# Kernel optimization log

Measured on AMD Instinct MI355X. Metric: run time of the kernel, lower is better.

Reference implementation:

```python
import jax, jax.numpy as jnp
import numpy as np

K_PRESERVE = 256
NUM_NEW = 1
UNITS = 768
HEAD_DIM = 64
N_HEADS = UNITS // HEAD_DIM
HID = 768


def setup_inputs() -> dict:
    key = jax.random.key(0)
    ks = jax.random.split(key, 12)
    B, H, L, D = 32, 12, 512, HID
    s = 0.02
    return {
        "hidden_states": jax.random.normal(ks[0], (B, L, D), jnp.float32),
        "attention_mask": jnp.zeros((B, 1, 1, L), jnp.float32),
        "self_attention_scores": jax.random.normal(ks[1], (B, H, L, L), jnp.float32),
        "Wq": jax.random.normal(ks[2], (D, UNITS), jnp.float32) * s,
        "bq": jnp.zeros((UNITS,), jnp.float32),
        "Wk": jax.random.normal(ks[3], (D, UNITS), jnp.float32) * s,
        "bk": jnp.zeros((UNITS,), jnp.float32),
        "Wv": jax.random.normal(ks[4], (D, UNITS), jnp.float32) * s,
        "bv": jnp.zeros((UNITS,), jnp.float32),
        "Wo": jax.random.normal(ks[5], (UNITS, D), jnp.float32) * s,
        "bo": jnp.zeros((D,), jnp.float32),
    }


def _forward(hidden_states, attention_mask, self_attention_scores,
             Wq, bq, Wk, bk, Wv, bv, Wo, bo):
    B, L, D = hidden_states.shape
    # K after reserving the new token slot
    K = max(min(K_PRESERVE, L) - NUM_NEW, 1)

    am = attention_mask.reshape(B, L)                      # additive mask as [B,L]
    amf = (am > -10.0).astype(jnp.float32)
    elem = amf[:, :, None] * amf[:, None, :]               # [B,L,L]
    scores = self_attention_scores * elem[:, None, :, :]   # [B,H,L,L]

    imp = scores.mean(axis=1).mean(axis=1)                 # [B,L]
    imp = imp.at[:, 0].set(jnp.inf)                        # always keep CLS
    _, idx = jax.lax.top_k(imp, K)                         # [B,K]
    idx = jnp.sort(idx, axis=-1)                           # boolean-mask gather keeps order

    preserved = jnp.take_along_axis(hidden_states, idx[:, :, None], axis=1)  # [B,K,D]
    preserved_mask = jnp.take_along_axis(am, idx, axis=1).reshape(B, 1, 1, K)

    # sentence vector = softmax(mask) @ hidden
    att = jax.nn.softmax(am, axis=-1)                      # [B,L]
    sentences = jnp.einsum('bl,bld->bd', att, hidden_states)[:, None, :]  # [B,1,D]
    key_pad = am < -10.0                                    # [B,L] True = masked

    # small cross-attention producing one new token
    q = (sentences @ Wq + bq).reshape(B, 1, N_HEADS, HEAD_DIM)
    k = (hidden_states @ Wk + bk).reshape(B, L, N_HEADS, HEAD_DIM)
    v = (hidden_states @ Wv + bv).reshape(B, L, N_HEADS, HEAD_DIM)
    logits = jnp.einsum('bqhd,blhd->bhql', q, k) / np.sqrt(HEAD_DIM).astype(np.float32)
    logits = jnp.where(key_pad[:, None, None, :], -jnp.inf, logits)
    w = jax.nn.softmax(logits, axis=-1)                    # [B,H,1,L]
    ctx = jnp.einsum('bhql,blhd->bqhd', w, v).reshape(B, 1, UNITS)
    new_token = ctx @ Wo + bo                              # [B,1,D]

    final_token = jnp.concatenate([preserved, new_token], axis=1)         # [B,K+1,D]
    new_mask = jnp.zeros((B, 1, 1, 1), jnp.float32)
    final_mask = jnp.concatenate([preserved_mask, new_mask], axis=-1)     # [B,1,1,K+1]
    tome_size = jnp.ones((B, K + 1, 1), jnp.float32)
    return final_token, final_mask, tome_size


def reference(hidden_states, attention_mask, self_attention_scores,
              Wq, bq, Wk, bk, Wv, bv, Wo, bo):
    return _forward(hidden_states, attention_mask, self_attention_scores,
                    Wq, bq, Wk, bk, Wv, bv, Wo, bo)
```

## Files before the change

### kernel.cpp

```cpp
#include <hip/hip_runtime.h>
#include <cstdint>
#include <cstddef>

#define B 32
#define H 12
#define L 512
#define D 768
#define KSEL 255

#define OFF_IMP   0
#define MEMSET_BYTES 65536
#define OFF_ATT   65536
#define OFF_SENT  131072
#define OFF_Q     229376
#define OFF_CB    327680
#define OFF_A     329216
#define OFF_LG    1508864
#define OFF_SEL   2295296
#define OFF_Y     2327936
#define OFF_CTX   3507584

__device__ __forceinline__ void imp_slice(const float* __restrict__ sas,
                                          const float* __restrict__ am,
                                          float* __restrict__ imp,
                                          int vb, int t, float4* red) {
  const int b = vb / 48, r = vb % 48, h = r >> 2, ch = r & 3;
  const int g = t >> 7, c = t & 127;
  const int row0 = ch * 128 + g * 32;
  const float* base = sas + (((size_t)(b * H + h)) * L + row0) * L;
  const float* amb = am + b * L + row0;
  float a0 = 0, a1 = 0, a2 = 0, a3 = 0;
#pragma unroll 8
  for (int l = 0; l < 32; ++l) {
    const float m = (amb[l] > -10.0f) ? 1.0f : 0.0f;
    const float4 v = reinterpret_cast<const float4*>(base + (size_t)l * L)[c];
    a0 += m * v.x;
    a1 += m * v.y;
    a2 += m * v.z;
    a3 += m * v.w;
  }
  red[g * 128 + c] = make_float4(a0, a1, a2, a3);
  __syncthreads();
  if (g == 0) {
    const float4 r0 = red[c], r1 = red[128 + c], r2 = red[256 + c], r3 = red[384 + c];
    float* ip = imp + b * L + c * 4;
    atomicAdd(ip + 0, r0.x + r1.x + r2.x + r3.x);
    atomicAdd(ip + 1, r0.y + r1.y + r2.y + r3.y);
    atomicAdd(ip + 2, r0.z + r1.z + r2.z + r3.z);
    atomicAdd(ip + 3, r0.w + r1.w + r2.w + r3.w);
  }
}

__global__ __launch_bounds__(512) void k_f1(const float* __restrict__ sas,
                                            const float* __restrict__ am,
                                            float* __restrict__ imp,
                                            float* __restrict__ att,
                                            float* __restrict__ sent) {
  __shared__ float4 red[512];
  __shared__ float r1[8], r2[8];
  const int bid = blockIdx.x, t = threadIdx.x;
  imp_slice(sas, am, imp, bid, t, red);
  if (bid < B) {
    const int b = bid, l = t;
    sent[b * D + l] = 0.0f;
    if (l < D - 512) sent[b * D + 512 + l] = 0.0f;
    const float aml = am[b * L + l];
    float m = aml;
#pragma unroll
    for (int o = 32; o; o >>= 1) m = fmaxf(m, __shfl_down(m, o));
    if ((l & 63) == 0) r1[l >> 6] = m;
    __syncthreads();
    if (l == 0) {
      float mm = r1[0];
      for (int i = 1; i < 8; ++i) mm = fmaxf(mm, r1[i]);
      r1[0] = mm;
    }
    __syncthreads();
    const float M = r1[0];
    const float e = expf(aml - M);
    float s = e;
#pragma unroll
    for (int o = 32; o; o >>= 1) s += __shfl_down(s, o);
    if ((l & 63) == 0) r2[l >> 6] = s;
    __syncthreads();
    if (l == 0) {
      float ss = 0.f;
      for (int i = 0; i < 8; ++i) ss += r2[i];
      r2[0] = ss;
    }
    __syncthreads();
    att[b * L + l] = e / r2[0];
  }
}

__global__ __launch_bounds__(512) void k_f2(const float* __restrict__ sas,
                                            const float* __restrict__ am,
                                            const float* __restrict__ hs,
                                            const float* __restrict__ att,
                                            float* __restrict__ imp,
                                            float* __restrict__ sent) {
  __shared__ float4 red[512];
  __shared__ float a[64];
  __shared__ float4 red2[8][192];
  const int bid = blockIdx.x, t = threadIdx.x;
  imp_slice(sas, am, imp, 512 + bid, t, red);
  if (bid < 256) {
    const int b = bid >> 3, c = bid & 7;
    const int w = t >> 6, lane = t & 63;
    if (t < 64) a[t] = att[b * L + c * 64 + t];
    __syncthreads();
    const float* h0 = hs + ((size_t)b * L + c * 64) * D;
    float4 s0 = {0, 0, 0, 0}, s1 = {0, 0, 0, 0}, s2 = {0, 0, 0, 0};
    for (int l = w; l < 64; l += 8) {
      const float al = a[l];
      const float4* row = reinterpret_cast<const float4*>(h0 + (size_t)l * D);
      const float4 v0 = row[lane], v1 = row[lane + 64], v2 = row[lane + 128];
      s0.x += al * v0.x; s0.y += al * v0.y; s0.z += al * v0.z; s0.w += al * v0.w;
      s1.x += al * v1.x; s1.y += al * v1.y; s1.z += al * v1.z; s1.w += al * v1.w;
      s2.x += al * v2.x; s2.y += al * v2.y; s2.z += al * v2.z; s2.w += al * v2.w;
    }
    red2[w][lane] = s0;
    red2[w][lane + 64] = s1;
    red2[w][lane + 128] = s2;
    __syncthreads();
    if (t < 192) {
      float4 s = {0, 0, 0, 0};
#pragma unroll
      for (int ww = 0; ww < 8; ++ww) {
        const float4 u = red2[ww][t];
        s.x += u.x; s.y += u.y; s.z += u.z; s.w += u.w;
      }
      float* sp = sent + b * D + t * 4;
      atomicAdd(sp + 0, s.x);
      atomicAdd(sp + 1, s.y);
      atomicAdd(sp + 2, s.z);
      atomicAdd(sp + 3, s.w);
    }
  }
}

__global__ __launch_bounds__(512) void k_f3(const float* __restrict__ sas,
                                            const float* __restrict__ am,
                                            const float* __restrict__ sent,
                                            const float* __restrict__ Wq,
                                            const float* __restrict__ bq,
                                            const float* __restrict__ bk,
                                            float* __restrict__ imp,
                                            float* __restrict__ qg,
                                            float* __restrict__ cbg,
                                            float* __restrict__ y) {
  __shared__ float4 red[512];
  const int bid = blockIdx.x, t = threadIdx.x;
  imp_slice(sas, am, imp, 1024 + bid, t, red);
  if (bid < 48) {
    const int h = bid >> 2;
    const int b = (bid & 3) * 8 + (t >> 6);
    const int ul = t & 63;
    const int u = h * 64 + ul;
    const float* sb = sent + b * D;
    float a0 = 0.f, a1 = 0.f, a2 = 0.f, a3 = 0.f;
#pragma unroll 4
    for (int d = 0; d < D; d += 4) {
      a0 += sb[d + 0] * Wq[(size_t)(d + 0) * D + u];
      a1 += sb[d + 1] * Wq[(size_t)(d + 1) * D + u];
      a2 += sb[d + 2] * Wq[(size_t)(d + 2) * D + u];
      a3 += sb[d + 3] * Wq[(size_t)(d + 3) * D + u];
    }
    const float acc = bq[u] + ((a0 + a1) + (a2 + a3));
    qg[b * D + u] = acc;
    float v = bk[u] * acc;
#pragma unroll
    for (int o = 32; o; o >>= 1) v += __shfl_down(v, o);
    if (ul == 0) cbg[b * H + h] = v;
  } else if (bid < 80) {
    const int b = bid - 48;
    for (int i = t; i < H * D; i += 512) y[(size_t)b * H * D + i] = 0.0f;
  }
}

__global__ __launch_bounds__(512) void k_f4(const float* __restrict__ am,
                                            const float* __restrict__ imp,
                                            const float* __restrict__ qg,
                                            const float* __restrict__ Wk,
                                            int* __restrict__ sel,
                                            float* __restrict__ out_mask,
                                            float* __restrict__ out_tome,
                                            float* __restrict__ Ag) {
  const int bid = blockIdx.x, t = threadIdx.x;
  __shared__ float v[512];
  __shared__ int sc[512];
  __shared__ float tile[64][65];
  if (bid < B) {
    const int b = bid, l = t;
    const float aml = am[b * L + l];
    float val;
    if (l == 0)
      val = INFINITY;
    else
      val = (aml > -10.0f) ? imp[b * L + l] : 0.0f;
    v[l] = val;
    __syncthreads();
    int r = 0;
    for (int tt = 0; tt < 512; ++tt) {
      const float vt = v[tt];
      r += (vt > val) || (vt == val && tt < l);
    }
    const int f = (r < KSEL) ? 1 : 0;
    sc[l] = f;
    __syncthreads();
    for (int off = 1; off < 512; off <<= 1) {
      const int add = (l >= off) ? sc[l - off] : 0;
      __syncthreads();
      sc[l] += add;
      __syncthreads();
    }
    if (f) {
      const int pos = sc[l] - 1;
      sel[b * KSEL + pos] = l;
      out_mask[b * 256 + pos] = aml;
    }
    if (l == 0) out_mask[b * 256 + 255] = 0.0f;
    if (l < 256) out_tome[b * 256 + l] = 1.0f;
  } else {
    const int vb = bid - B;
    const int h = vb / 12, dc = vb % 12;
    for (int i = t; i < 4096; i += 512) {
      const int rr = i >> 6, cc = i & 63;
      tile[rr][cc] = Wk[(size_t)(dc * 64 + rr) * D + h * 64 + cc];
    }
    __syncthreads();
    const int dl = t & 63, bl = t >> 6;
    const int d = dc * 64 + dl;
#pragma unroll
    for (int pass = 0; pass < 4; ++pass) {
      const int b = pass * 8 + bl;
      const float* qh = qg + b * D + h * 64;
      float acc = 0.f;
#pragma unroll
      for (int c = 0; c < 64; ++c) acc += tile[dl][c] * qh[c];
      Ag[((size_t)b * H + h) * D + d] = acc;
    }
  }
}

__global__ __launch_bounds__(256) void k_f5(const float* __restrict__ hs,
                                            const float* __restrict__ Ag,
                                            const float* __restrict__ cbg,
                                            const int* __restrict__ sel,
                                            float* __restrict__ lg,
                                            float* __restrict__ out_tok) {
  const int bid = blockIdx.x, t = threadIdx.x;
  __shared__ float A[H * D];
  if (bid < 512) {
    const int b = bid >> 4, ch = bid & 15;
    for (int i = t; i < H * D; i += 256) A[i] = Ag[(size_t)b * H * D + i];
    __syncthreads();
    const int wave = t >> 6, lane = t & 63;
    const float* h0 = hs + (size_t)b * L * D;
    for (int li = 0; li < 8; ++li) {
      const int l = ch * 32 + li * 4 + wave;
      const float* xr = h0 + (size_t)l * D;
      float xv[12];
#pragma unroll
      for (int k = 0; k < 12; ++k) xv[k] = xr[lane + 64 * k];
#pragma unroll
      for (int h = 0; h < H; ++h) {
        float a = 0.f;
#pragma unroll
        for (int k = 0; k < 12; ++k) a += xv[k] * A[h * D + lane + 64 * k];
#pragma unroll
        for (int o = 32; o; o >>= 1) a += __shfl_down(a, o);
        if (lane == 0) lg[((size_t)b * H + h) * L + l] = (a + cbg[b * H + h]) * 0.125f;
      }
    }
  } else {
    const int vb = bid - 512;
    const int row = vb * 4 + (t >> 6);
    const int lane = t & 63;
    const int b = row / KSEL, p = row % KSEL;
    const int j = sel[row];
    const float4* src = reinterpret_cast<const float4*>(hs + ((size_t)b * L + j) * D);
    float4* dst = reinterpret_cast<float4*>(out_tok + ((size_t)b * 256 + p) * D);
#pragma unroll
    for (int i = 0; i < 3; ++i) dst[lane + 64 * i] = src[lane + 64 * i];
  }
}

__global__ __launch_bounds__(768) void k_ysoft(const float* __restrict__ hs,
                                               const float* __restrict__ lg,
                                               const float* __restrict__ am,
                                               float* __restrict__ y) {
  const int b = blockIdx.x, c = blockIdx.y, t = threadIdx.x;
  __shared__ float wl[H * L];
  __shared__ float Ms[H], Is[H];
  __shared__ float wn[H * 64];
  for (int i = t; i < H * L; i += 768) {
    const int l = i & (L - 1);
    const float aml = am[b * L + l];
    wl[i] = (aml < -10.0f) ? -INFINITY : lg[(size_t)b * H * L + i];
  }
  __syncthreads();
  {
    const int h = t >> 6, lane = t & 63;
    float m = -INFINITY;
#pragma unroll
    for (int k = 0; k < 8; ++k) m = fmaxf(m, wl[h * L + lane + 64 * k]);
#pragma unroll
    for (int o = 32; o; o >>= 1) m = fmaxf(m, __shfl_xor(m, o));
    float s = 0.f;
#pragma unroll
    for (int k = 0; k < 8; ++k) s += expf(wl[h * L + lane + 64 * k] - m);
#pragma unroll
    for (int o = 32; o; o >>= 1) s += __shfl_xor(s, o);
    if (lane == 0) { Ms[h] = m; Is[h] = 1.0f / s; }
  }
  __syncthreads();
  {
    const int h = t >> 6, l = t & 63;
    wn[t] = expf(wl[h * L + c * 64 + l] - Ms[h]) * Is[h];
  }
  __syncthreads();
  const float* h0 = hs + ((size_t)b * L + c * 64) * D;
  float acc[12];
#pragma unroll
  for (int h = 0; h < 12; ++h) acc[h] = 0.f;
  for (int l = 0; l < 64; ++l) {
    const float x = h0[(size_t)l * D + t];
#pragma unroll
    for (int h = 0; h < 12; ++h) acc[h] += wn[h * 64 + l] * x;
  }
#pragma unroll
  for (int h = 0; h < 12; ++h) atomicAdd(&y[((size_t)b * H + h) * D + t], acc[h]);
}

__global__ __launch_bounds__(512) void k_ctx(const float* __restrict__ y,
                                             const float* __restrict__ Wv,
                                             const float* __restrict__ bv,
                                             float* __restrict__ ctx) {
  const int h = blockIdx.x;
  const int b = blockIdx.y * 8 + (threadIdx.x >> 6);
  const int c = threadIdx.x & 63;
  const float* yb = y + ((size_t)b * H + h) * D;
  float a0 = 0.f, a1 = 0.f, a2 = 0.f, a3 = 0.f;
#pragma unroll 4
  for (int d = 0; d < D; d += 4) {
    a0 += yb[d + 0] * Wv[(size_t)(d + 0) * D + h * 64 + c];
    a1 += yb[d + 1] * Wv[(size_t)(d + 1) * D + h * 64 + c];
    a2 += yb[d + 2] * Wv[(size_t)(d + 2) * D + h * 64 + c];
    a3 += yb[d + 3] * Wv[(size_t)(d + 3) * D + h * 64 + c];
  }
  ctx[b * D + h * 64 + c] = bv[h * 64 + c] + ((a0 + a1) + (a2 + a3));
}

__global__ __launch_bounds__(512) void k_out(const float* __restrict__ ctx,
                                             const float* __restrict__ Wo,
                                             const float* __restrict__ bo,
                                             float* __restrict__ out_tok) {
  const int dc = blockIdx.x;
  const int b = blockIdx.y * 8 + (threadIdx.x >> 6);
  const int dl = threadIdx.x & 63;
  const int dd = dc * 64 + dl;
  const float* cb = ctx + b * D;
  float a0 = 0.f, a1 = 0.f, a2 = 0.f, a3 = 0.f;
#pragma unroll 4
  for (int u = 0; u < D; u += 4) {
    a0 += cb[u + 0] * Wo[(size_t)(u + 0) * D + dd];
    a1 += cb[u + 1] * Wo[(size_t)(u + 1) * D + dd];
    a2 += cb[u + 2] * Wo[(size_t)(u + 2) * D + dd];
    a3 += cb[u + 3] * Wo[(size_t)(u + 3) * D + dd];
  }
  out_tok[((size_t)b * 256 + 255) * D + dd] = bo[dd] + ((a0 + a1) + (a2 + a3));
}

extern "C" void kernel_launch(void* const* d_in, const int* in_sizes, int n_in,
                              void* d_out, int out_size, void* d_ws, size_t ws_size,
                              hipStream_t stream) {
  const float* hs = (const float*)d_in[0];
  const float* am = (const float*)d_in[1];
  const float* sas = (const float*)d_in[2];
  const float* Wq = (const float*)d_in[3];
  const float* bq = (const float*)d_in[4];
  const float* Wk = (const float*)d_in[5];
  const float* bk = (const float*)d_in[6];
  const float* Wv = (const float*)d_in[7];
  const float* bv = (const float*)d_in[8];
  const float* Wo = (const float*)d_in[9];
  const float* bo = (const float*)d_in[10];

  float* out_tok = (float*)d_out;
  float* out_mask = out_tok + (size_t)B * 256 * D;
  float* out_tome = out_mask + (size_t)B * 256;

  char* ws = (char*)d_ws;
  float* imp = (float*)(ws + OFF_IMP);
  float* att = (float*)(ws + OFF_ATT);
  float* sent = (float*)(ws + OFF_SENT);
  float* qg = (float*)(ws + OFF_Q);
  float* cbg = (float*)(ws + OFF_CB);
  float* Ag = (float*)(ws + OFF_A);
  float* lg = (float*)(ws + OFF_LG);
  int* sel = (int*)(ws + OFF_SEL);
  float* yg = (float*)(ws + OFF_Y);
  float* ctx = (float*)(ws + OFF_CTX);

  hipMemsetAsync(d_ws, 0, MEMSET_BYTES, stream);

  k_f1<<<512, 512, 0, stream>>>(sas, am, imp, att, sent);
  k_f2<<<512, 512, 0, stream>>>(sas, am, hs, att, imp, sent);
  k_f3<<<512, 512, 0, stream>>>(sas, am, sent, Wq, bq, bk, imp, qg, cbg, yg);
  k_f4<<<176, 512, 0, stream>>>(am, imp, qg, Wk, sel, out_mask, out_tome, Ag);
  k_f5<<<2552, 256, 0, stream>>>(hs, Ag, cbg, sel, lg, out_tok);
  k_ysoft<<<dim3(B, 8), 768, 0, stream>>>(hs, lg, am, yg);
  k_ctx<<<dim3(12, 4), 512, 0, stream>>>(yg, Wv, bv, ctx);
  k_out<<<dim3(12, 4), 512, 0, stream>>>(ctx, Wo, bo, out_tok);
}
```

Measured before the change: 751.3 us.

## Merge all stages into one cooperative persistent kernel with grid syncs

Replaces the memset and eight separate kernel launches with a single cooperative kernel of 256 blocks of 768 threads that uses grid-wide syncs between phases. The importance reduction over the score tensor is re-tiled per (batch, head) and interleaved with the sentence-vector and Q/A projections. The ctx and output projections are fused per batch through shared memory. This removes launch gaps and inter-kernel bubbles, but restricts parallelism to 256 resident blocks and adds grid-sync overhead, which may underuse bandwidth on the large score read.

```diff
diff --git a/kernel.cpp b/kernel.cpp
--- a/kernel.cpp
+++ b/kernel.cpp
@@ -1,37 +1,47 @@
 #include <hip/hip_runtime.h>
+#include <hip/hip_cooperative_groups.h>
 #include <cstdint>
 #include <cstddef>
+
+namespace cg = cooperative_groups;
 
 #define B 32
 #define H 12
 #define L 512
 #define D 768
 #define KSEL 255
+#define GN 256
+#define NT 768
 
 #define OFF_IMP   0
-#define MEMSET_BYTES 65536
-#define OFF_ATT   65536
-#define OFF_SENT  131072
-#define OFF_Q     229376
-#define OFF_CB    327680
-#define OFF_A     329216
-#define OFF_LG    1508864
-#define OFF_SEL   2295296
-#define OFF_Y     2327936
-#define OFF_CTX   3507584
-
-__device__ __forceinline__ void imp_slice(const float* __restrict__ sas,
-                                          const float* __restrict__ am,
-                                          float* __restrict__ imp,
-                                          int vb, int t, float4* red) {
-  const int b = vb / 48, r = vb % 48, h = r >> 2, ch = r & 3;
+#define OFF_SENT  65536
+#define OFF_Y     163840
+#define ZERO_F4   83968
+#define OFF_CB    1343488
+#define OFF_A     1345024
+#define OFF_LG    2524672
+#define OFF_SEL   3311104
+
+union ShMem {
+  struct { float4 red[768]; } imp;
+  struct { float4 red2[12][192]; float r1[8]; float r2[8]; float a[64]; } sent;
+  struct { float qpart[12][64]; float q_s[64]; } qa;
+  struct { float v[512]; int sc[512]; } prep;
+  struct { float wl[H * L]; float Ms[H]; float Is[H]; float wn[NT]; } ys;
+  struct { float c[D]; } ctxout;
+};
+
+__device__ __forceinline__ void imp_vb(const float* __restrict__ sas,
+                                       const float* __restrict__ am,
+                                       float* __restrict__ imp,
+                                       int vb, int t, float4* red) {
+  const int b = vb / H, h = vb % H;
   const int g = t >> 7, c = t & 127;
-  const int row0 = ch * 128 + g * 32;
-  const float* base = sas + (((size_t)(b * H + h)) * L + row0) * L;
-  const float* amb = am + b * L + row0;
-  float a0 = 0, a1 = 0, a2 = 0, a3 = 0;
-#pragma unroll 8
-  for (int l = 0; l < 32; ++l) {
+  const float* base = sas + ((size_t)(b * H + h)) * L * L;
+  const float* amb = am + b * L;
+  float a0 = 0.f, a1 = 0.f, a2 = 0.f, a3 = 0.f;
+#pragma unroll 4
+  for (int l = g; l < L; l += 6) {
     const float m = (amb[l] > -10.0f) ? 1.0f : 0.0f;
     const float4 v = reinterpret_cast<const float4*>(base + (size_t)l * L)[c];
     a0 += m * v.x;
@@ -39,337 +49,300 @@
     a2 += m * v.z;
     a3 += m * v.w;
   }
-  red[g * 128 + c] = make_float4(a0, a1, a2, a3);
+  red[t] = make_float4(a0, a1, a2, a3);
   __syncthreads();
   if (g == 0) {
-    const float4 r0 = red[c], r1 = red[128 + c], r2 = red[256 + c], r3 = red[384 + c];
+    float4 s = red[c];
+#pragma unroll
+    for (int gg = 1; gg < 6; ++gg) {
+      const float4 u = red[gg * 128 + c];
+      s.x += u.x; s.y += u.y; s.z += u.z; s.w += u.w;
+    }
     float* ip = imp + b * L + c * 4;
-    atomicAdd(ip + 0, r0.x + r1.x + r2.x + r3.x);
-    atomicAdd(ip + 1, r0.y + r1.y + r2.y + r3.y);
-    atomicAdd(ip + 2, r0.z + r1.z + r2.z + r3.z);
-    atomicAdd(ip + 3, r0.w + r1.w + r2.w + r3.w);
-  }
-}
-
-__global__ __launch_bounds__(512) void k_f1(const float* __restrict__ sas,
-                                            const float* __restrict__ am,
-                                            float* __restrict__ imp,
-                                            float* __restrict__ att,
-                                            float* __restrict__ sent) {
-  __shared__ float4 red[512];
-  __shared__ float r1[8], r2[8];
+    atomicAdd(ip + 0, s.x);
+    atomicAdd(ip + 1, s.y);
+    atomicAdd(ip + 2, s.z);
+    atomicAdd(ip + 3, s.w);
+  }
+  __syncthreads();
+}
+
+__device__ __forceinline__ void sent_unit(const float* __restrict__ am,
+                                          const float* __restrict__ hs,
+                                          float* __restrict__ sent,
+                                          int u, int t, ShMem& sh) {
+  const int b = u >> 3, c = u & 7;
+  const int w = t >> 6, lane = t & 63;
+  const float aml = (t < L) ? am[b * L + t] : -INFINITY;
+  float m = aml;
+#pragma unroll
+  for (int o = 32; o; o >>= 1) m = fmaxf(m, __shfl_down(m, o));
+  if (t < L && lane == 0) sh.sent.r1[w] = m;
+  __syncthreads();
+  if (t == 0) {
+    float mm = sh.sent.r1[0];
+    for (int i = 1; i < 8; ++i) mm = fmaxf(mm, sh.sent.r1[i]);
+    sh.sent.r1[0] = mm;
+  }
+  __syncthreads();
+  const float M = sh.sent.r1[0];
+  const float e = (t < L) ? expf(aml - M) : 0.f;
+  float s = e;
+#pragma unroll
+  for (int o = 32; o; o >>= 1) s += __shfl_down(s, o);
+  if (t < L && lane == 0) sh.sent.r2[w] = s;
+  __syncthreads();
+  if (t == 0) {
+    float ss = 0.f;
+    for (int i = 0; i < 8; ++i) ss += sh.sent.r2[i];
+    sh.sent.r2[0] = ss;
+  }
+  __syncthreads();
+  const float S = sh.sent.r2[0];
+  if (t >= c * 64 && t < c * 64 + 64) sh.sent.a[t - c * 64] = e / S;
+  __syncthreads();
+  const float* h0 = hs + ((size_t)b * L + c * 64) * D;
+  float4 s0 = {0, 0, 0, 0}, s1 = {0, 0, 0, 0}, s2 = {0, 0, 0, 0};
+  for (int l = w; l < 64; l += 12) {
+    const float al = sh.sent.a[l];
+    const float4* row = reinterpret_cast<const float4*>(h0 + (size_t)l * D);
+    const float4 v0 = row[lane], v1 = row[lane + 64], v2 = row[lane + 128];
+    s0.x += al * v0.x; s0.y += al * v0.y; s0.z += al * v0.z; s0.w += al * v0.w;
+    s1.x += al * v1.x; s1.y += al * v1.y; s1.z += al * v1.z; s1.w += al * v1.w;
+    s2.x += al * v2.x; s2.y += al * v2.y; s2.z += al * v2.z; s2.w += al * v2.w;
+  }
+  sh.sent.red2[w][lane] = s0;
+  sh.sent.red2[w][lane + 64] = s1;
+  sh.sent.red2[w][lane + 128] = s2;
+  __syncthreads();
+  if (t < 192) {
+    float4 acc = {0, 0, 0, 0};
+#pragma unroll
+    for (int ww = 0; ww < 12; ++ww) {
+      const float4 uu = sh.sent.red2[ww][t];
+      acc.x += uu.x; acc.y += uu.y; acc.z += uu.z; acc.w += uu.w;
+    }
+    float* sp = sent + b * D + t * 4;
+    atomicAdd(sp + 0, acc.x);
+    atomicAdd(sp + 1, acc.y);
+    atomicAdd(sp + 2, acc.z);
+    atomicAdd(sp + 3, acc.w);
+  }
+  __syncthreads();
+}
+
+__device__ __forceinline__ void qa_unit(const float* __restrict__ sent,
+                                        const float* __restrict__ Wq,
+                                        const float* __restrict__ bq,
+                                        const float* __restrict__ bk,
+                                        const float* __restrict__ Wk,
+                                        float* __restrict__ cbg,
+                                        float* __restrict__ Ag,
+                                        int u, int t, ShMem& sh) {
+  const int b = u / H, h = u % H;
+  const int w = t >> 6, lane = t & 63;
+  const float* sb = sent + b * D;
+  const float* wq = Wq + (size_t)(w * 64) * D + h * 64 + lane;
+  float acc = 0.f;
+#pragma unroll 8
+  for (int dd = 0; dd < 64; ++dd) acc += sb[w * 64 + dd] * wq[(size_t)dd * D];
+  sh.qa.qpart[w][lane] = acc;
+  __syncthreads();
+  if (t < 64) {
+    float q = bq[h * 64 + t];
+#pragma unroll
+    for (int ww = 0; ww < 12; ++ww) q += sh.qa.qpart[ww][t];
+    sh.qa.q_s[t] = q;
+  }
+  __syncthreads();
+  if (t < 64) {
+    float v = bk[h * 64 + t] * sh.qa.q_s[t];
+#pragma unroll
+    for (int o = 32; o; o >>= 1) v += __shfl_down(v, o);
+    if (t == 0) cbg[b * H + h] = v;
+  }
+  const float4* wkrow = reinterpret_cast<const float4*>(Wk + (size_t)t * D + h * 64);
+  float a0 = 0.f, a1 = 0.f, a2 = 0.f, a3 = 0.f;
+#pragma unroll
+  for (int cc = 0; cc < 16; ++cc) {
+    const float4 wv = wkrow[cc];
+    a0 += wv.x * sh.qa.q_s[cc * 4 + 0];
+    a1 += wv.y * sh.qa.q_s[cc * 4 + 1];
+    a2 += wv.z * sh.qa.q_s[cc * 4 + 2];
+    a3 += wv.w * sh.qa.q_s[cc * 4 + 3];
+  }
+  Ag[((size_t)b * H + h) * D + t] = (a0 + a1) + (a2 + a3);
+  __syncthreads();
+}
+
+__global__ __launch_bounds__(NT, 3) void k_mega(
+    const float* __restrict__ hs, const float* __restrict__ am,
+    const float* __restrict__ sas,
+    const float* __restrict__ Wq, const float* __restrict__ bq,
+    const float* __restrict__ Wk, const float* __restrict__ bk,
+    const float* __restrict__ Wv, const float* __restrict__ bv,
+    const float* __restrict__ Wo, const float* __restrict__ bo,
+    float* __restrict__ imp, float* __restrict__ sent, float* __restrict__ y,
+    float* __restrict__ cbg, float* __restrict__ Ag, float* __restrict__ lg,
+    int* __restrict__ sel, float* __restrict__ out_tok,
+    float* __restrict__ out_mask, float* __restrict__ out_tome) {
+  cg::grid_group grid = cg::this_grid();
+  __shared__ ShMem sh;
   const int bid = blockIdx.x, t = threadIdx.x;
-  imp_slice(sas, am, imp, bid, t, red);
+
+  {
+    const int gtid = bid * NT + t;
+    float4* zz = reinterpret_cast<float4*>(imp);
+    if (gtid < ZERO_F4) zz[gtid] = make_float4(0.f, 0.f, 0.f, 0.f);
+    if (gtid < B * 256) out_tome[gtid] = 1.0f;
+    if (gtid < B) out_mask[gtid * 256 + 255] = 0.0f;
+  }
+  grid.sync();
+
+  if (bid < 192) {
+    imp_vb(sas, am, imp, bid, t, sh.imp.red);
+  } else {
+    for (int k = 0; k < 4; ++k) sent_unit(am, hs, sent, (bid - 192) + 64 * k, t, sh);
+  }
+  grid.sync();
+
+  if (bid >= 64) {
+    imp_vb(sas, am, imp, 192 + (bid - 64), t, sh.imp.red);
+  } else {
+    for (int k = 0; k < 6; ++k) qa_unit(sent, Wq, bq, bk, Wk, cbg, Ag, bid + 64 * k, t, sh);
+  }
+  grid.sync();
+
   if (bid < B) {
-    const int b = bid, l = t;
-    sent[b * D + l] = 0.0f;
-    if (l < D - 512) sent[b * D + 512 + l] = 0.0f;
-    const float aml = am[b * L + l];
-    float m = aml;
-#pragma unroll
-    for (int o = 32; o; o >>= 1) m = fmaxf(m, __shfl_down(m, o));
-    if ((l & 63) == 0) r1[l >> 6] = m;
-    __syncthreads();
-    if (l == 0) {
-      float mm = r1[0];
-      for (int i = 1; i < 8; ++i) mm = fmaxf(mm, r1[i]);
-      r1[0] = mm;
-    }
-    __syncthreads();
-    const float M = r1[0];
-    const float e = expf(aml - M);
-    float s = e;
-#pragma unroll
-    for (int o = 32; o; o >>= 1) s += __shfl_down(s, o);
-    if ((l & 63) == 0) r2[l >> 6] = s;
-    __syncthreads();
-    if (l == 0) {
-      float ss = 0.f;
-      for (int i = 0; i < 8; ++i) ss += r2[i];
-      r2[0] = ss;
-    }
-    __syncthreads();
-    att[b * L + l] = e / r2[0];
-  }
-}
-
-__global__ __launch_bounds__(512) void k_f2(const float* __restrict__ sas,
-                                            const float* __restrict__ am,
-                                            const float* __restrict__ hs,
-                                            const float* __restrict__ att,
-                                            float* __restrict__ imp,
-                                            float* __restrict__ sent) {
-  __shared__ float4 red[512];
-  __shared__ float a[64];
-  __shared__ float4 red2[8][192];
-  const int bid = blockIdx.x, t = threadIdx.x;
-  imp_slice(sas, am, imp, 512 + bid, t, red);
-  if (bid < 256) {
+    const int b = bid;
+    float aml = 0.f, val = 0.f;
+    if (t < L) {
+      aml = am[b * L + t];
+      val = (t == 0) ? INFINITY : ((aml > -10.0f) ? imp[b * L + t] : 0.0f);
+      sh.prep.v[t] = val;
+    }
+    __syncthreads();
+    int r = 0;
+    if (t < L) {
+      for (int tt = 0; tt < L; ++tt) {
+        const float vt = sh.prep.v[tt];
+        r += (vt > val) || (vt == val && tt < t);
+      }
+      sh.prep.sc[t] = (r < KSEL) ? 1 : 0;
+    }
+    const int f = (t < L) && (r < KSEL);
+    __syncthreads();
+    for (int off = 1; off < L; off <<= 1) {
+      int add = 0;
+      if (t < L && t >= off) add = sh.prep.sc[t - off];
+      __syncthreads();
+      if (t < L) sh.prep.sc[t] += add;
+      __syncthreads();
+    }
+    if (f) {
+      const int pos = sh.prep.sc[t] - 1;
+      sel[b * KSEL + pos] = t;
+      out_mask[b * 256 + pos] = aml;
+    }
+  } else {
+    const int h = t >> 6, lane = t & 63;
+    for (int u = bid - 32; u < B * 16; u += 224) {
+      const int b = u >> 4, ch = u & 15;
+      const float cbh = cbg[b * H + h];
+      float Areg[12];
+#pragma unroll
+      for (int k = 0; k < 12; ++k) Areg[k] = Ag[((size_t)b * H + h) * D + lane + 64 * k];
+      const float* h0 = hs + (size_t)b * L * D;
+      for (int li = 0; li < 32; ++li) {
+        const int l = ch * 32 + li;
+        const float* xr = h0 + (size_t)l * D;
+        float a = 0.f;
+#pragma unroll
+        for (int k = 0; k < 12; ++k) a += xr[lane + 64 * k] * Areg[k];
+#pragma unroll
+        for (int o = 32; o; o >>= 1) a += __shfl_down(a, o);
+        if (lane == 0) lg[((size_t)b * H + h) * L + l] = (a + cbh) * 0.125f;
+      }
+    }
+  }
+  grid.sync();
+
+  {
     const int b = bid >> 3, c = bid & 7;
+    for (int i = t; i < H * L; i += NT) {
+      const int l = i & (L - 1);
+      const float aml = am[b * L + l];
+      sh.ys.wl[i] = (aml < -10.0f) ? -INFINITY : lg[(size_t)b * H * L + i];
+    }
+    __syncthreads();
+    {
+      const int h = t >> 6, lane = t & 63;
+      float m = -INFINITY;
+#pragma unroll
+      for (int k = 0; k < 8; ++k) m = fmaxf(m, sh.ys.wl[h * L + lane + 64 * k]);
+#pragma unroll
+      for (int o = 32; o; o >>= 1) m = fmaxf(m, __shfl_xor(m, o));
+      float s = 0.f;
+#pragma unroll
+      for (int k = 0; k < 8; ++k) s += expf(sh.ys.wl[h * L + lane + 64 * k] - m);
+#pragma unroll
+      for (int o = 32; o; o >>= 1) s += __shfl_xor(s, o);
+      if (lane == 0) { sh.ys.Ms[h] = m; sh.ys.Is[h] = 1.0f / s; }
+    }
+    __syncthreads();
+    {
+      const int h = t >> 6, l = t & 63;
+      sh.ys.wn[t] = expf(sh.ys.wl[h * L + c * 64 + l] - sh.ys.Ms[h]) * sh.ys.Is[h];
+    }
+    __syncthreads();
+    const float* h0 = hs + ((size_t)b * L + c * 64) * D;
+    float acc[12];
+#pragma unroll
+    for (int h = 0; h < 12; ++h) acc[h] = 0.f;
+    for (int l = 0; l < 64; ++l) {
+      const float x = h0[(size_t)l * D + t];
+#pragma unroll
+      for (int h = 0; h < 12; ++h) acc[h] += sh.ys.wn[h * 64 + l] * x;
+    }
+#pragma unroll
+    for (int h = 0; h < 12; ++h) atomicAdd(&y[((size_t)b * H + h) * D + t], acc[h]);
+  }
+  {
     const int w = t >> 6, lane = t & 63;
-    if (t < 64) a[t] = att[b * L + c * 64 + t];
-    __syncthreads();
-    const float* h0 = hs + ((size_t)b * L + c * 64) * D;
-    float4 s0 = {0, 0, 0, 0}, s1 = {0, 0, 0, 0}, s2 = {0, 0, 0, 0};
-    for (int l = w; l < 64; l += 8) {
-      const float al = a[l];
-      const float4* row = reinterpret_cast<const float4*>(h0 + (size_t)l * D);
-      const float4 v0 = row[lane], v1 = row[lane + 64], v2 = row[lane + 128];
-      s0.x += al * v0.x; s0.y += al * v0.y; s0.z += al * v0.z; s0.w += al * v0.w;
-      s1.x += al * v1.x; s1.y += al * v1.y; s1.z += al * v1.z; s1.w += al * v1.w;
-      s2.x += al * v2.x; s2.y += al * v2.y; s2.z += al * v2.z; s2.w += al * v2.w;
-    }
-    red2[w][lane] = s0;
-    red2[w][lane + 64] = s1;
-    red2[w][lane + 128] = s2;
-    __syncthreads();
-    if (t < 192) {
-      float4 s = {0, 0, 0, 0};
-#pragma unroll
-      for (int ww = 0; ww < 8; ++ww) {
-        const float4 u = red2[ww][t];
-        s.x += u.x; s.y += u.y; s.z += u.z; s.w += u.w;
-      }
-      float* sp = sent + b * D + t * 4;
-      atomicAdd(sp + 0, s.x);
-      atomicAdd(sp + 1, s.y);
-      atomicAdd(sp + 2, s.z);
-      atomicAdd(sp + 3, s.w);
-    }
-  }
-}
-
-__global__ __launch_bounds__(512) void k_f3(const float* __restrict__ sas,
-                                            const float* __restrict__ am,
-                                            const float* __restrict__ sent,
-                                            const float* __restrict__ Wq,
-                                            const float* __restrict__ bq,
-                                            const float* __restrict__ bk,
-                                            float* __restrict__ imp,
-                                            float* __restrict__ qg,
-                                            float* __restrict__ cbg,
-                                            float* __restrict__ y) {
-  __shared__ float4 red[512];
-  const int bid = blockIdx.x, t = threadIdx.x;
-  imp_slice(sas, am, imp, 1024 + bid, t, red);
-  if (bid < 48) {
-    const int h = bid >> 2;
-    const int b = (bid & 3) * 8 + (t >> 6);
-    const int ul = t & 63;
-    const int u = h * 64 + ul;
-    const float* sb = sent + b * D;
+    for (int rr = bid * 12 + w; rr < B * KSEL; rr += GN * 12) {
+      const int b2 = rr / KSEL, p = rr % KSEL;
+      const int j = sel[rr];
+      const float4* src = reinterpret_cast<const float4*>(hs + ((size_t)b2 * L + j) * D);
+      float4* dst = reinterpret_cast<float4*>(out_tok + ((size_t)b2 * 256 + p) * D);
+#pragma unroll
+      for (int i = 0; i < 3; ++i) dst[lane + 64 * i] = src[lane + 64 * i];
+    }
+  }
+  grid.sync();
+
+  if (bid < B) {
+    const int b = bid;
+    const float* yh = y + ((size_t)b * H + (t >> 6)) * D;
     float a0 = 0.f, a1 = 0.f, a2 = 0.f, a3 = 0.f;
 #pragma unroll 4
     for (int d = 0; d < D; d += 4) {
-      a0 += sb[d + 0] * Wq[(size_t)(d + 0) * D + u];
-      a1 += sb[d + 1] * Wq[(size_t)(d + 1) * D + u];
-      a2 += sb[d + 2] * Wq[(size_t)(d + 2) * D + u];
-      a3 += sb[d + 3] * Wq[(size_t)(d + 3) * D + u];
-    }
-    const float acc = bq[u] + ((a0 + a1) + (a2 + a3));
-    qg[b * D + u] = acc;
-    float v = bk[u] * acc;
-#pragma unroll
-    for (int o = 32; o; o >>= 1) v += __shfl_down(v, o);
-    if (ul == 0) cbg[b * H + h] = v;
-  } else if (bid < 80) {
-    const int b = bid - 48;
-    for (int i = t; i < H * D; i += 512) y[(size_t)b * H * D + i] = 0.0f;
-  }
-}
-
-__global__ __launch_bounds__(512) void k_f4(const float* __restrict__ am,
-                                            const float* __restrict__ imp,
-                                            const float* __restrict__ qg,
-                                            const float* __restrict__ Wk,
-                                            int* __restrict__ sel,
-                                            float* __restrict__ out_mask,
-                                            float* __restrict__ out_tome,
-                                            float* __restrict__ Ag) {
-  const int bid = blockIdx.x, t = threadIdx.x;
-  __shared__ float v[512];
-  __shared__ int sc[512];
-  __shared__ float tile[64][65];
-  if (bid < B) {
-    const int b = bid, l = t;
-    const float aml = am[b * L + l];
-    float val;
-    if (l == 0)
-      val = INFINITY;
-    else
-      val = (aml > -10.0f) ? imp[b * L + l] : 0.0f;
-    v[l] = val;
-    __syncthreads();
-    int r = 0;
-    for (int tt = 0; tt < 512; ++tt) {
-      const float vt = v[tt];
-      r += (vt > val) || (vt == val && tt < l);
-    }
-    const int f = (r < KSEL) ? 1 : 0;
-    sc[l] = f;
-    __syncthreads();
-    for (int off = 1; off < 512; off <<= 1) {
-      const int add = (l >= off) ? sc[l - off] : 0;
-      __syncthreads();
-      sc[l] += add;
-      __syncthreads();
-    }
-    if (f) {
-      const int pos = sc[l] - 1;
-      sel[b * KSEL + pos] = l;
-      out_mask[b * 256 + pos] = aml;
-    }
-    if (l == 0) out_mask[b * 256 + 255] = 0.0f;
-    if (l < 256) out_tome[b * 256 + l] = 1.0f;
-  } else {
-    const int vb = bid - B;
-    const int h = vb / 12, dc = vb % 12;
-    for (int i = t; i < 4096; i += 512) {
-      const int rr = i >> 6, cc = i & 63;
-      tile[rr][cc] = Wk[(size_t)(dc * 64 + rr) * D + h * 64 + cc];
-    }
-    __syncthreads();
-    const int dl = t & 63, bl = t >> 6;
-    const int d = dc * 64 + dl;
-#pragma unroll
-    for (int pass = 0; pass < 4; ++pass) {
-      const int b = pass * 8 + bl;
-      const float* qh = qg + b * D + h * 64;
-      float acc = 0.f;
-#pragma unroll
-      for (int c = 0; c < 64; ++c) acc += tile[dl][c] * qh[c];
-      Ag[((size_t)b * H + h) * D + d] = acc;
-    }
-  }
-}
-
-__global__ __launch_bounds__(256) void k_f5(const float* __restrict__ hs,
-                                            const float* __restrict__ Ag,
-                                            const float* __restrict__ cbg,
-                                            const int* __restrict__ sel,
-                                            float* __restrict__ lg,
-                                            float* __restrict__ out_tok) {
-  const int bid = blockIdx.x, t = threadIdx.x;
-  __shared__ float A[H * D];
-  if (bid < 512) {
-    const int b = bid >> 4, ch = bid & 15;
-    for (int i = t; i < H * D; i += 256) A[i] = Ag[(size_t)b * H * D + i];
-    __syncthreads();
-    const int wave = t >> 6, lane = t & 63;
-    const float* h0 = hs + (size_t)b * L * D;
-    for (int li = 0; li < 8; ++li) {
-      const int l = ch * 32 + li * 4 + wave;
-      const float* xr = h0 + (size_t)l * D;
-      float xv[12];
-#pragma unroll
-      for (int k = 0; k < 12; ++k) xv[k] = xr[lane + 64 * k];
-#pragma unroll
-      for (int h = 0; h < H; ++h) {
-        float a = 0.f;
-#pragma unroll
-        for (int k = 0; k < 12; ++k) a += xv[k] * A[h * D + lane + 64 * k];
-#pragma unroll
-        for (int o = 32; o; o >>= 1) a += __shfl_down(a, o);
-        if (lane == 0) lg[((size_t)b * H + h) * L + l] = (a + cbg[b * H + h]) * 0.125f;
-      }
-    }
-  } else {
-    const int vb = bid - 512;
-    const int row = vb * 4 + (t >> 6);
-    const int lane = t & 63;
-    const int b = row / KSEL, p = row % KSEL;
-    const int j = sel[row];
-    const float4* src = reinterpret_cast<const float4*>(hs + ((size_t)b * L + j) * D);
-    float4* dst = reinterpret_cast<float4*>(out_tok + ((size_t)b * 256 + p) * D);
-#pragma unroll
-    for (int i = 0; i < 3; ++i) dst[lane + 64 * i] = src[lane + 64 * i];
-  }
-}
-
-__global__ __launch_bounds__(768) void k_ysoft(const float* __restrict__ hs,
-                                               const float* __restrict__ lg,
-                                               const float* __restrict__ am,
-                                               float* __restrict__ y) {
-  const int b = blockIdx.x, c = blockIdx.y, t = threadIdx.x;
-  __shared__ float wl[H * L];
-  __shared__ float Ms[H], Is[H];
-  __shared__ float wn[H * 64];
-  for (int i = t; i < H * L; i += 768) {
-    const int l = i & (L - 1);
-    const float aml = am[b * L + l];
-    wl[i] = (aml < -10.0f) ? -INFINITY : lg[(size_t)b * H * L + i];
-  }
-  __syncthreads();
-  {
-    const int h = t >> 6, lane = t & 63;
-    float m = -INFINITY;
-#pragma unroll
-    for (int k = 0; k < 8; ++k) m = fmaxf(m, wl[h * L + lane + 64 * k]);
-#pragma unroll
-    for (int o = 32; o; o >>= 1) m = fmaxf(m, __shfl_xor(m, o));
-    float s = 0.f;
-#pragma unroll
-    for (int k = 0; k < 8; ++k) s += expf(wl[h * L + lane + 64 * k] - m);
-#pragma unroll
-    for (int o = 32; o; o >>= 1) s += __shfl_xor(s, o);
-    if (lane == 0) { Ms[h] = m; Is[h] = 1.0f / s; }
-  }
-  __syncthreads();
-  {
-    const int h = t >> 6, l = t & 63;
-    wn[t] = expf(wl[h * L + c * 64 + l] - Ms[h]) * Is[h];
-  }
-  __syncthreads();
-  const float* h0 = hs + ((size_t)b * L + c * 64) * D;
-  float acc[12];
-#pragma unroll
-  for (int h = 0; h < 12; ++h) acc[h] = 0.f;
-  for (int l = 0; l < 64; ++l) {
-    const float x = h0[(size_t)l * D + t];
-#pragma unroll
-    for (int h = 0; h < 12; ++h) acc[h] += wn[h * 64 + l] * x;
-  }
-#pragma unroll
-  for (int h = 0; h < 12; ++h) atomicAdd(&y[((size_t)b * H + h) * D + t], acc[h]);
-}
-
-__global__ __launch_bounds__(512) void k_ctx(const float* __restrict__ y,
-                                             const float* __restrict__ Wv,
-                                             const float* __restrict__ bv,
-                                             float* __restrict__ ctx) {
-  const int h = blockIdx.x;
-  const int b = blockIdx.y * 8 + (threadIdx.x >> 6);
-  const int c = threadIdx.x & 63;
-  const float* yb = y + ((size_t)b * H + h) * D;
-  float a0 = 0.f, a1 = 0.f, a2 = 0.f, a3 = 0.f;
+      a0 += yh[d + 0] * Wv[(size_t)(d + 0) * D + t];
+      a1 += yh[d + 1] * Wv[(size_t)(d + 1) * D + t];
+      a2 += yh[d + 2] * Wv[(size_t)(d + 2) * D + t];
+      a3 += yh[d + 3] * Wv[(size_t)(d + 3) * D + t];
+    }
+    sh.ctxout.c[t] = bv[t] + ((a0 + a1) + (a2 + a3));
+    __syncthreads();
+    float b0 = 0.f, b1 = 0.f, b2 = 0.f, b3 = 0.f;
 #pragma unroll 4
-  for (int d = 0; d < D; d += 4) {
-    a0 += yb[d + 0] * Wv[(size_t)(d + 0) * D + h * 64 + c];
-    a1 += yb[d + 1] * Wv[(size_t)(d + 1) * D + h * 64 + c];
-    a2 += yb[d + 2] * Wv[(size_t)(d + 2) * D + h * 64 + c];
-    a3 += yb[d + 3] * Wv[(size_t)(d + 3) * D + h * 64 + c];
-  }
-  ctx[b * D + h * 64 + c] = bv[h * 64 + c] + ((a0 + a1) + (a2 + a3));
-}
-
-__global__ __launch_bounds__(512) void k_out(const float* __restrict__ ctx,
-                                             const float* __restrict__ Wo,
-                                             const float* __restrict__ bo,
-                                             float* __restrict__ out_tok) {
-  const int dc = blockIdx.x;
-  const int b = blockIdx.y * 8 + (threadIdx.x >> 6);
-  const int dl = threadIdx.x & 63;
-  const int dd = dc * 64 + dl;
-  const float* cb = ctx + b * D;
-  float a0 = 0.f, a1 = 0.f, a2 = 0.f, a3 = 0.f;
-#pragma unroll 4
-  for (int u = 0; u < D; u += 4) {
-    a0 += cb[u + 0] * Wo[(size_t)(u + 0) * D + dd];
-    a1 += cb[u + 1] * Wo[(size_t)(u + 1) * D + dd];
-    a2 += cb[u + 2] * Wo[(size_t)(u + 2) * D + dd];
-    a3 += cb[u + 3] * Wo[(size_t)(u + 3) * D + dd];
-  }
-  out_tok[((size_t)b * 256 + 255) * D + dd] = bo[dd] + ((a0 + a1) + (a2 + a3));
+    for (int u2 = 0; u2 < D; u2 += 4) {
+      b0 += sh.ctxout.c[u2 + 0] * Wo[(size_t)(u2 + 0) * D + t];
+      b1 += sh.ctxout.c[u2 + 1] * Wo[(size_t)(u2 + 1) * D + t];
+      b2 += sh.ctxout.c[u2 + 2] * Wo[(size_t)(u2 + 2) * D + t];
+      b3 += sh.ctxout.c[u2 + 3] * Wo[(size_t)(u2 + 3) * D + t];
+    }
+    out_tok[((size_t)b * 256 + 255) * D + t] = bo[t] + ((b0 + b1) + (b2 + b3));
+  }
 }
 
 extern "C" void kernel_launch(void* const* d_in, const int* in_sizes, int n_in,
@@ -393,24 +366,17 @@
 
   char* ws = (char*)d_ws;
   float* imp = (float*)(ws + OFF_IMP);
-  float* att = (float*)(ws + OFF_ATT);
   float* sent = (float*)(ws + OFF_SENT);
-  float* qg = (float*)(ws + OFF_Q);
+  float* yg = (float*)(ws + OFF_Y);
   float* cbg = (float*)(ws + OFF_CB);
   float* Ag = (float*)(ws + OFF_A);
   float* lg = (float*)(ws + OFF_LG);
   int* sel = (int*)(ws + OFF_SEL);
-  float* yg = (float*)(ws + OFF_Y);
-  float* ctx = (float*)(ws + OFF_CTX);
-
-  hipMemsetAsync(d_ws, 0, MEMSET_BYTES, stream);
-
-  k_f1<<<512, 512, 0, stream>>>(sas, am, imp, att, sent);
-  k_f2<<<512, 512, 0, stream>>>(sas, am, hs, att, imp, sent);
-  k_f3<<<512, 512, 0, stream>>>(sas, am, sent, Wq, bq, bk, imp, qg, cbg, yg);
-  k_f4<<<176, 512, 0, stream>>>(am, imp, qg, Wk, sel, out_mask, out_tome, Ag);
-  k_f5<<<2552, 256, 0, stream>>>(hs, Ag, cbg, sel, lg, out_tok);
-  k_ysoft<<<dim3(B, 8), 768, 0, stream>>>(hs, lg, am, yg);
-  k_ctx<<<dim3(12, 4), 512, 0, stream>>>(yg, Wv, bv, ctx);
-  k_out<<<dim3(12, 4), 512, 0, stream>>>(ctx, Wo, bo, out_tok);
-}
+
+  void* args[] = {(void*)&hs, (void*)&am, (void*)&sas, (void*)&Wq, (void*)&bq,
+                  (void*)&Wk, (void*)&bk, (void*)&Wv, (void*)&bv, (void*)&Wo,
+                  (void*)&bo, (void*)&imp, (void*)&sent, (void*)&yg, (void*)&cbg,
+                  (void*)&Ag, (void*)&lg, (void*)&sel, (void*)&out_tok,
+                  (void*)&out_mask, (void*)&out_tome};
+  hipLaunchCooperativeKernel((void*)k_mega, dim3(GN), dim3(NT), args, 0, stream);
+}
```

Result: slower. 920.5 us (+22.5%).
